# Kernel tuning notes

Hardware: AMD Instinct MI355X
Metric: run time of the kernel (lower is better)

Reference implementation:

```python
import jax, jax.numpy as jnp
import numpy as np

DIM = 1024
N_HEAD = 16
N_KV_HEAD = 4
HEAD_DIM = DIM // N_HEAD  # 64
INTER = 2688
B, N = 2, 2048
EPS = 1e-6


def setup_inputs() -> dict:
    key = jax.random.key(0)
    ks = jax.random.split(key, 10)
    std = 0.02
    x = jax.random.normal(ks[0], (B, N, DIM), dtype=jnp.float32)
    # rotary embedding: theta = pos * 10000^(-2i/d), cos/sin of shape [N, HEAD_DIM//2]
    inv_freq = 1.0 / (10000.0 ** (np.arange(0, HEAD_DIM, 2, dtype=np.float32) / HEAD_DIM))
    t = np.arange(N, dtype=np.float32)
    ang = np.outer(t, inv_freq)  # [N, HEAD_DIM//2]
    rope_cos = jnp.asarray(np.cos(ang))
    rope_sin = jnp.asarray(np.sin(ang))
    mask = jnp.tril(jnp.ones((N, N), dtype=bool))  # True = attend
    return {
        "x": x,
        "w_attn_norm": jnp.ones((DIM,), jnp.float32),
        "w_ffn_norm": jnp.ones((DIM,), jnp.float32),
        "Wq": jax.random.normal(ks[1], (DIM, N_HEAD * HEAD_DIM), jnp.float32) * std,
        "Wkv": jax.random.normal(ks[2], (DIM, 2 * N_KV_HEAD * HEAD_DIM), jnp.float32) * std,
        "Wo": jax.random.normal(ks[3], (N_HEAD * HEAD_DIM, DIM), jnp.float32) * std,
        "W1": jax.random.normal(ks[4], (DIM, INTER), jnp.float32) * std,
        "W2": jax.random.normal(ks[5], (INTER, DIM), jnp.float32) * std,
        "W3": jax.random.normal(ks[6], (DIM, INTER), jnp.float32) * std,
        "rope_cos": rope_cos,
        "rope_sin": rope_sin,
        "mask": mask,
    }


def _rms_norm(x, w):
    # nn.functional.rms_norm: x / sqrt(mean(x^2) + eps) * w
    return x * jax.lax.rsqrt(jnp.mean(x * x, axis=-1, keepdims=True) + EPS) * w


def _apply_rope(x, cos, sin):
    # x: [b, n, h, d]; consecutive pairs (x[2k], x[2k+1]) form complex numbers
    xr = x[..., 0::2]
    xi = x[..., 1::2]
    c = cos[None, :, None, :]
    s = sin[None, :, None, :]
    yr = xr * c - xi * s
    yi = xr * s + xi * c
    return jnp.stack([yr, yi], axis=-1).reshape(x.shape)


def _block(x, w_attn_norm, w_ffn_norm, Wq, Wkv, Wo, W1, W2, W3, rope_cos, rope_sin, mask):
    b, n, _ = x.shape
    # --- attention (GQA, use_cache=False prefill) ---
    h = _rms_norm(x, w_attn_norm)
    q = (h @ Wq).reshape(b, n, N_HEAD, HEAD_DIM)
    kv = h @ Wkv
    k, v = jnp.split(kv, 2, axis=-1)
    k = k.reshape(b, n, N_KV_HEAD, HEAD_DIM)
    v = v.reshape(b, n, N_KV_HEAD, HEAD_DIM)
    q = _apply_rope(q, rope_cos, rope_sin)
    k = _apply_rope(k, rope_cos, rope_sin)
    # einops repeat 'b n h d -> b n (r h) d' == tile along head axis
    r = N_HEAD // N_KV_HEAD
    k = jnp.tile(k, (1, 1, r, 1))
    v = jnp.tile(v, (1, 1, r, 1))
    scale = HEAD_DIM ** -0.5
    scores = jnp.einsum('bnhd,bmhd->bhnm', q, k) * scale
    scores = jnp.where(mask[None, None, :, :], scores, jnp.finfo(scores.dtype).min)
    attn = jax.nn.softmax(scores, axis=-1)
    o = jnp.einsum('bhnm,bmhd->bnhd', attn, v).reshape(b, n, N_HEAD * HEAD_DIM)
    x = x + o @ Wo
    # --- SwiGLU MLP ---
    h2 = _rms_norm(x, w_ffn_norm)
    ff = (jax.nn.silu(h2 @ W1) * (h2 @ W3)) @ W2
    return x + ff


def reference(x, w_attn_norm, w_ffn_norm, Wq, Wkv, Wo, W1, W2, W3, rope_cos, rope_sin, mask):
    return _block(x, w_attn_norm, w_ffn_norm, Wq, Wkv, Wo, W1, W2, W3, rope_cos, rope_sin, mask)
```

## Files before the change

kernel.cpp:

```cpp
#include <hip/hip_runtime.h>

#define DIM 1024
#define NH 16
#define NKV 4
#define HD 64
#define INTER 2688
#define BB 2
#define NN 2048
#define MM (BB*NN)

typedef __attribute__((ext_vector_type(4))) float f32x4;
typedef __attribute__((ext_vector_type(16))) float f32x16;
typedef __attribute__((ext_vector_type(8))) short short8;

#define CROW(r,h) ((((r)&3)) + 8*((r)>>2) + 4*(h))

__device__ __forceinline__ unsigned short f2bf(float f) {
  union { float f; unsigned u; } v; v.f = f;
  unsigned r = v.u + 0x7fffu + ((v.u >> 16) & 1u);
  return (unsigned short)(r >> 16);
}
__device__ __forceinline__ float bf2f(unsigned short u) {
  union { unsigned u; float f; } v; v.u = ((unsigned)u) << 16; return v.f;
}
__device__ __forceinline__ float ld_res(const float* p) { return *p; }
__device__ __forceinline__ float ld_res(const unsigned short* p) { return bf2f(*p); }
__device__ __forceinline__ void st_out(float* p, float v) { *p = v; }
__device__ __forceinline__ void st_out(unsigned short* p, float v) { *p = f2bf(v); }

__device__ __forceinline__ void glds16(const unsigned short* g, unsigned short* l) {
  __builtin_amdgcn_global_load_lds(
      (const __attribute__((address_space(1))) void*)g,
      (__attribute__((address_space(3))) void*)l, 16, 0, 0);
}

__device__ __forceinline__ void xcd_map(int& bx, int& by) {
  int gx = gridDim.x;
  int nwg = gx * gridDim.y;
  int bid = (int)blockIdx.y * gx + (int)blockIdx.x;
  int cpx = nwg >> 3;
  int lg = (bid & 7) * cpx + (bid >> 3);
  bx = lg % gx;
  by = lg / gx;
}

__global__ void transpose_all(const float* __restrict__ Wq, const float* __restrict__ Wkv,
                              const float* __restrict__ Wo, const float* __restrict__ W1,
                              const float* __restrict__ W3, const float* __restrict__ W2,
                              unsigned short* __restrict__ WqkvT, unsigned short* __restrict__ WoT,
                              unsigned short* __restrict__ W1T, unsigned short* __restrict__ W3T,
                              unsigned short* __restrict__ W2T) {
  int tb = blockIdx.x;
  const float* src; unsigned short* dst; int K, Nc, t0;
  if (tb < 1024)        { src = Wq;  dst = WqkvT;                         K = 1024; Nc = 1024; t0 = tb; }
  else if (tb < 1536)   { src = Wkv; dst = WqkvT + (size_t)1024 * 1024;   K = 1024; Nc = 512;  t0 = tb - 1024; }
  else if (tb < 2560)   { src = Wo;  dst = WoT;                           K = 1024; Nc = 1024; t0 = tb - 1536; }
  else if (tb < 5248)   { src = W1;  dst = W1T;                           K = 1024; Nc = 2688; t0 = tb - 2560; }
  else if (tb < 7936)   { src = W3;  dst = W3T;                           K = 1024; Nc = 2688; t0 = tb - 5248; }
  else                  { src = W2;  dst = W2T;                           K = 2688; Nc = 1024; t0 = tb - 7936; }
  int ntx = Nc >> 5;
  int n0 = (t0 % ntx) * 32, k0 = (t0 / ntx) * 32;
  __shared__ float tile[32][33];
  int tx = threadIdx.x & 31, ty = threadIdx.x >> 5;
#pragma unroll
  for (int i = 0; i < 32; i += 8)
    tile[ty + i][tx] = src[(size_t)(k0 + ty + i) * Nc + n0 + tx];
  __syncthreads();
#pragma unroll
  for (int i = 0; i < 32; i += 8)
    dst[(size_t)(n0 + ty + i) * K + k0 + tx] = f2bf(tile[tx][ty + i]);
}

template <typename InT>
__global__ void rmsnorm_k(const InT* __restrict__ x, const float* __restrict__ w,
                          unsigned short* __restrict__ h) {
  int row = blockIdx.x;
  int t = threadIdx.x;
  float4 v;
  if constexpr (sizeof(InT) == 4) {
    v = ((const float4*)(x + (size_t)row * DIM))[t];
  } else {
    ushort4 u = ((const ushort4*)(x + (size_t)row * DIM))[t];
    v.x = bf2f(u.x); v.y = bf2f(u.y); v.z = bf2f(u.z); v.w = bf2f(u.w);
  }
  float ss = v.x * v.x + v.y * v.y + v.z * v.z + v.w * v.w;
#pragma unroll
  for (int o = 1; o < 64; o <<= 1) ss += __shfl_xor(ss, o);
  __shared__ float ps[4];
  if ((t & 63) == 0) ps[t >> 6] = ss;
  __syncthreads();
  float r = rsqrtf((ps[0] + ps[1] + ps[2] + ps[3]) * (1.0f / DIM) + 1e-6f);
  float4 wv = ((const float4*)w)[t];
  ushort4 o4;
  o4.x = f2bf(v.x * r * wv.x);
  o4.y = f2bf(v.y * r * wv.y);
  o4.z = f2bf(v.z * r * wv.z);
  o4.w = f2bf(v.w * r * wv.w);
  *(ushort4*)(h + (size_t)row * DIM + t * 4) = o4;
}

template <typename ResT, typename OutT>
__global__ __launch_bounds__(256, 3) void gemm64(
    const unsigned short* __restrict__ A, const unsigned short* __restrict__ Bt,
    const ResT* __restrict__ res, OutT* __restrict__ C, int Nc, int K) {
  __shared__ __align__(16) unsigned short Asm[2][64 * 64];
  __shared__ __align__(16) unsigned short Bsm[2][128 * 64];
  int tid = threadIdx.x;
  int w = tid >> 6, l = tid & 63;
  int bx, by;
  xcd_map(bx, by);
  int bm = by * 64, bn = bx * 128;
  int wc = w * 32;
  int c0 = l & 15, g = l >> 4;

  int sra = w * 16 + (l >> 3);
  int srb = w * 32 + (l >> 3);
  int schA = ((l & 7) ^ (l >> 3)) * 8;
  const unsigned short* gA = A + (size_t)(bm + sra) * K + schA;
  const unsigned short* gB = Bt + (size_t)(bn + srb) * K + schA;
  int lsa = (w * 16) * 64, lsb = (w * 32) * 64;

  f32x4 acc[4][2] = {};
  int T = K / 64;
  glds16(gA, &Asm[0][lsa]);
  glds16(gA + 8 * K, &Asm[0][lsa + 8 * 64]);
  glds16(gB, &Bsm[0][lsb]);
  glds16(gB + 8 * K, &Bsm[0][lsb + 8 * 64]);
  glds16(gB + 16 * K, &Bsm[0][lsb + 16 * 64]);
  glds16(gB + 24 * K, &Bsm[0][lsb + 24 * 64]);
  __syncthreads();
  int buf = 0;
  for (int s = 0; s < T; ++s) {
    int nb = buf ^ 1;
    if (s + 1 < T) {
      int ko = (s + 1) * 64;
      glds16(gA + ko, &Asm[nb][lsa]);
      glds16(gA + 8 * K + ko, &Asm[nb][lsa + 8 * 64]);
      glds16(gB + ko, &Bsm[nb][lsb]);
      glds16(gB + 8 * K + ko, &Bsm[nb][lsb + 8 * 64]);
      glds16(gB + 16 * K + ko, &Bsm[nb][lsb + 16 * 64]);
      glds16(gB + 24 * K + ko, &Bsm[nb][lsb + 24 * 64]);
    }
    const unsigned short* As = Asm[buf];
    const unsigned short* Bs = Bsm[buf];
#pragma unroll
    for (int ks = 0; ks < 2; ++ks) {
      short8 af[4], bf[2];
#pragma unroll
      for (int m = 0; m < 4; m++) {
        int ra = m * 16 + c0;
        af[m] = *(const short8*)&As[ra * 64 + (((ks * 4 + g) ^ (ra & 7)) * 8)];
      }
#pragma unroll
      for (int n = 0; n < 2; n++) {
        int rb = wc + n * 16 + c0;
        bf[n] = *(const short8*)&Bs[rb * 64 + (((ks * 4 + g) ^ (rb & 7)) * 8)];
      }
      __builtin_amdgcn_s_setprio(1);
#pragma unroll
      for (int m = 0; m < 4; m++)
#pragma unroll
        for (int n = 0; n < 2; n++)
          acc[m][n] = __builtin_amdgcn_mfma_f32_16x16x32_bf16(af[m], bf[n], acc[m][n], 0, 0, 0);
      __builtin_amdgcn_s_setprio(0);
    }
    __syncthreads();
    buf = nb;
  }
  int gq = l >> 4;
#pragma unroll
  for (int m = 0; m < 4; m++) {
#pragma unroll
    for (int i = 0; i < 4; i++) {
      int row = bm + m * 16 + gq * 4 + i;
#pragma unroll
      for (int n = 0; n < 2; n++) {
        int col = bn + wc + n * 16 + c0;
        float v = acc[m][n][i] + ld_res(&res[(size_t)row * Nc + col]);
        st_out(&C[(size_t)row * Nc + col], v);
      }
    }
  }
}

__global__ __launch_bounds__(256, 3) void gemm_qkv(
    const unsigned short* __restrict__ A, const unsigned short* __restrict__ Bt,
    const float* __restrict__ cosb, const float* __restrict__ sinb,
    unsigned short* __restrict__ qb, unsigned short* __restrict__ kb,
    unsigned short* __restrict__ vtb) {
  const int K = 1024;
  const float QS = 0.125f * 1.44269504f;
  __shared__ __align__(16) unsigned short Asm[2][64 * 64];
  __shared__ __align__(16) unsigned short Bsm[2][128 * 64];
  int tid = threadIdx.x;
  int w = tid >> 6, l = tid & 63;
  int bx, by;
  xcd_map(bx, by);
  int bm = by * 64, bn = bx * 128;
  int wc = w * 32;
  int c0 = l & 15, g = l >> 4;

  int sra = w * 16 + (l >> 3);
  int srb = w * 32 + (l >> 3);
  int schA = ((l & 7) ^ (l >> 3)) * 8;
  const unsigned short* gA = A + (size_t)(bm + sra) * K + schA;
  const unsigned short* gB = Bt + (size_t)(bn + srb) * K + schA;
  int lsa = (w * 16) * 64, lsb = (w * 32) * 64;

  f32x4 acc[4][2] = {};
  int T = K / 64;
  glds16(gA, &Asm[0][lsa]);
  glds16(gA + 8 * K, &Asm[0][lsa + 8 * 64]);
  glds16(gB, &Bsm[0][lsb]);
  glds16(gB + 8 * K, &Bsm[0][lsb + 8 * 64]);
  glds16(gB + 16 * K, &Bsm[0][lsb + 16 * 64]);
  glds16(gB + 24 * K, &Bsm[0][lsb + 24 * 64]);
  __syncthreads();
  int buf = 0;
  for (int s = 0; s < T; ++s) {
    int nb = buf ^ 1;
    if (s + 1 < T) {
      int ko = (s + 1) * 64;
      glds16(gA + ko, &Asm[nb][lsa]);
      glds16(gA + 8 * K + ko, &Asm[nb][lsa + 8 * 64]);
      glds16(gB + ko, &Bsm[nb][lsb]);
      glds16(gB + 8 * K + ko, &Bsm[nb][lsb + 8 * 64]);
      glds16(gB + 16 * K + ko, &Bsm[nb][lsb + 16 * 64]);
      glds16(gB + 24 * K + ko, &Bsm[nb][lsb + 24 * 64]);
    }
    const unsigned short* As = Asm[buf];
    const unsigned short* Bs = Bsm[buf];
#pragma unroll
    for (int ks = 0; ks < 2; ++ks) {
      short8 af[4], bf[2];
#pragma unroll
      for (int m = 0; m < 4; m++) {
        int ra = m * 16 + c0;
        af[m] = *(const short8*)&As[ra * 64 + (((ks * 4 + g) ^ (ra & 7)) * 8)];
      }
#pragma unroll
      for (int n = 0; n < 2; n++) {
        int rb = wc + n * 16 + c0;
        bf[n] = *(const short8*)&Bs[rb * 64 + (((ks * 4 + g) ^ (rb & 7)) * 8)];
      }
      __builtin_amdgcn_s_setprio(1);
#pragma unroll
      for (int m = 0; m < 4; m++)
#pragma unroll
        for (int n = 0; n < 2; n++)
          acc[m][n] = __builtin_amdgcn_mfma_f32_16x16x32_bf16(af[m], bf[n], acc[m][n], 0, 0, 0);
      __builtin_amdgcn_s_setprio(0);
    }
    __syncthreads();
    buf = nb;
  }
  int gq = l >> 4;
  int lodd = c0 & 1;
#pragma unroll
  for (int m = 0; m < 4; m++) {
#pragma unroll
    for (int i = 0; i < 4; i++) {
      int row = bm + m * 16 + gq * 4 + i;
      int b = row >> 11, tok = row & (NN - 1);
#pragma unroll
      for (int n = 0; n < 2; n++) {
        int col = bn + wc + n * 16 + c0;
        float val = acc[m][n][i];
        float partner = __shfl_xor(val, 1);
        if (bn < 1024) {
          int head = col >> 6, d = col & 63, j = d >> 1;
          float c = cosb[tok * 32 + j], s = sinb[tok * 32 + j];
          float r = lodd ? (partner * s + val * c) : (val * c - partner * s);
          qb[(((size_t)(b * NH + head)) * NN + tok) * 64 + d] = f2bf(r * QS);
        } else if (bn < 1280) {
          int cc = col - 1024;
          int kvh = cc >> 6, d = cc & 63, j = d >> 1;
          float c = cosb[tok * 32 + j], s = sinb[tok * 32 + j];
          float r = lodd ? (partner * s + val * c) : (val * c - partner * s);
          kb[(((size_t)(b * NKV + kvh)) * NN + tok) * 64 + d] = f2bf(r);
        } else {
          int cc = col - 1280;
          int kvh = cc >> 6, d = cc & 63;
          vtb[(((size_t)(b * NKV + kvh)) * 64 + d) * NN + tok] = f2bf(val);
        }
      }
    }
  }
}

__global__ __launch_bounds__(256, 4) void gemm_ffn13(
    const unsigned short* __restrict__ A, const unsigned short* __restrict__ B1t,
    const unsigned short* __restrict__ B3t, unsigned short* __restrict__ G,
    int Nc, int K) {
  __shared__ __align__(16) unsigned short Asm[2 * 128 * 32];
  __shared__ __align__(16) unsigned short B1sm[2 * 64 * 32];
  __shared__ __align__(16) unsigned short B3sm[2 * 64 * 32];
  int tid = threadIdx.x;
  int w = tid >> 6, l = tid & 63;
  int bm = blockIdx.y * 128, bn = blockIdx.x * 64;
  int wr = (w >> 1) * 64, wc = (w & 1) * 32;
  int c0 = l & 15, g = l >> 4;

  int sr = w * 32 + (l >> 2);
  int sb = w * 16 + (l >> 2);
  int sc  = ((l & 3) ^ ((sr >> 1) & 3)) * 8;
  int scb = ((l & 3) ^ ((sb >> 1) & 3)) * 8;
  const unsigned short* gA0 = A + (size_t)(bm + sr) * K + sc;
  const unsigned short* gA1 = A + (size_t)(bm + sr + 16) * K + sc;
  const unsigned short* gB1 = B1t + (size_t)(bn + sb) * K + scb;
  const unsigned short* gB3 = B3t + (size_t)(bn + sb) * K + scb;
  int ls0 = (w * 32) * 32, ls1 = (w * 32 + 16) * 32, lsb = (w * 16) * 32;

  int aoff[4], boff[2];
#pragma unroll
  for (int m = 0; m < 4; m++) {
    int ra = wr + m * 16 + c0;
    aoff[m] = ra * 32 + (g ^ ((ra >> 1) & 3)) * 8;
  }
#pragma unroll
  for (int n = 0; n < 2; n++) {
    int rb = wc + n * 16 + c0;
    boff[n] = rb * 32 + (g ^ ((rb >> 1) & 3)) * 8;
  }

  f32x4 a1[4][2] = {};
  f32x4 a3[4][2] = {};
  int nsteps = K / 32;
  glds16(gA0, &Asm[ls0]);
  glds16(gA1, &Asm[ls1]);
  glds16(gB1, &B1sm[lsb]);
  glds16(gB3, &B3sm[lsb]);
  __syncthreads();
  int buf = 0;
  for (int s = 0; s < nsteps; ++s) {
    int nb = buf ^ 1;
    if (s + 1 < nsteps) {
      int ko = (s + 1) * 32;
      glds16(gA0 + ko, &Asm[nb * 4096 + ls0]);
      glds16(gA1 + ko, &Asm[nb * 4096 + ls1]);
      glds16(gB1 + ko, &B1sm[nb * 2048 + lsb]);
      glds16(gB3 + ko, &B3sm[nb * 2048 + lsb]);
    }
    const unsigned short* As = &Asm[buf * 4096];
    const unsigned short* B1s = &B1sm[buf * 2048];
    const unsigned short* B3s = &B3sm[buf * 2048];
    short8 af[4], b1f[2], b3f[2];
#pragma unroll
    for (int m = 0; m < 4; m++) af[m] = *(const short8*)&As[aoff[m]];
#pragma unroll
    for (int n = 0; n < 2; n++) {
      b1f[n] = *(const short8*)&B1s[boff[n]];
      b3f[n] = *(const short8*)&B3s[boff[n]];
    }
    __builtin_amdgcn_s_setprio(1);
#pragma unroll
    for (int m = 0; m < 4; m++)
#pragma unroll
      for (int n = 0; n < 2; n++) {
        a1[m][n] = __builtin_amdgcn_mfma_f32_16x16x32_bf16(af[m], b1f[n], a1[m][n], 0, 0, 0);
        a3[m][n] = __builtin_amdgcn_mfma_f32_16x16x32_bf16(af[m], b3f[n], a3[m][n], 0, 0, 0);
      }
    __builtin_amdgcn_s_setprio(0);
    __syncthreads();
    buf = nb;
  }
  int gq = l >> 4;
#pragma unroll
  for (int m = 0; m < 4; m++) {
#pragma unroll
    for (int i = 0; i < 4; i++) {
      int row = bm + wr + m * 16 + gq * 4 + i;
#pragma unroll
      for (int n = 0; n < 2; n++) {
        int col = bn + wc + n * 16 + c0;
        float x1 = a1[m][n][i], x3 = a3[m][n][i];
        float sg = x1 / (1.0f + __expf(-x1));
        G[(size_t)row * Nc + col] = f2bf(sg * x3);
      }
    }
  }
}

__global__ __launch_bounds__(256, 3) void attn_k(
    const unsigned short* __restrict__ qg_, const unsigned short* __restrict__ kg_,
    const unsigned short* __restrict__ vg_, unsigned short* __restrict__ ob) {
  __shared__ __align__(16) unsigned short Ksm[2][64 * 64];
  __shared__ __align__(16) unsigned short Vsm[2][64 * 64];
  int qb = (blockIdx.z == 0) ? (int)blockIdx.x : ((int)gridDim.x - 1 - (int)blockIdx.x);
  int h = blockIdx.y, b = blockIdx.z;
  int kvh = h & 3;
  int tid = threadIdx.x, w = tid >> 6, l = tid & 63;
  int q5 = l & 31, hi = l >> 5;
  int qwbase = qb * 128 + w * 32;
  int qgl = qwbase + q5;

  const unsigned short* Kg = kg_ + ((size_t)(b * NKV + kvh)) * NN * 64;
  const unsigned short* Vg = vg_ + ((size_t)(b * NKV + kvh)) * 64 * NN;

  short8 qf[4];
  {
    const unsigned short* qrow = qg_ + (((size_t)(b * NH + h)) * NN + qgl) * 64 + hi * 8;
#pragma unroll
    for (int d = 0; d < 4; d++) qf[d] = *(const short8*)(qrow + d * 16);
  }

  int srow = l >> 3;
  int schunk = (l & 7) ^ (srow & 7);
  const unsigned short* gK = Kg + (size_t)(w * 16 + srow) * 64 + schunk * 8;
  const unsigned short* gV = Vg + (size_t)(w * 16 + srow) * NN + schunk * 8;

  int nkt = qb * 2 + 2;
  int nkt_w = ((qwbase + 31) >> 6) + 1;

  f32x16 O0 = {}, O1 = {};
  float m_r = -1e30f, l_r = 0.0f;

  glds16(gK, &Ksm[0][w * 1024]);
  glds16(gK + 8 * 64, &Ksm[0][w * 1024 + 512]);
  glds16(gV, &Vsm[0][w * 1024]);
  glds16(gV + 8 * NN, &Vsm[0][w * 1024 + 512]);
  __syncthreads();

  int buf = 0;
  for (int kt = 0; kt < nkt; ++kt) {
    int n0 = kt * 64;
    if (kt + 1 < nkt) {
      int nb = buf ^ 1;
      glds16(gK + (size_t)(n0 + 64) * 64, &Ksm[nb][w * 1024]);
      glds16(gK + (size_t)(n0 + 64) * 64 + 8 * 64, &Ksm[nb][w * 1024 + 512]);
      glds16(gV + n0 + 64, &Vsm[nb][w * 1024]);
      glds16(gV + 8 * NN + n0 + 64, &Vsm[nb][w * 1024 + 512]);
    }
    if (kt < nkt_w) {
      const unsigned short* Ks = Ksm[buf];
      const unsigned short* Vs = Vsm[buf];
      f32x16 S[2];
      __builtin_amdgcn_s_setprio(1);
#pragma unroll
      for (int s = 0; s < 2; s++) {
        f32x16 acc = {};
        int row = s * 32 + q5;
#pragma unroll
        for (int d = 0; d < 4; d++) {
          int ch = (2 * d + hi) ^ (row & 7);
          short8 kf = *(const short8*)&Ks[row * 64 + ch * 8];
          acc = __builtin_amdgcn_mfma_f32_32x32x16_bf16(kf, qf[d], acc, 0, 0, 0);
        }
        S[s] = acc;
      }
      __builtin_amdgcn_s_setprio(0);
      if (kt == nkt_w - 1) {
#pragma unroll
        for (int s = 0; s < 2; s++)
#pragma unroll
          for (int r = 0; r < 16; r++) {
            int kg = n0 + s * 32 + CROW(r, hi);
            S[s][r] = (kg > qgl) ? -1e30f : S[s][r];
          }
      }
      float t16[16];
#pragma unroll
      for (int r = 0; r < 16; r++) t16[r] = fmaxf(S[0][r], S[1][r]);
#pragma unroll
      for (int k = 8; k >= 1; k >>= 1)
#pragma unroll
        for (int r = 0; r < k; r++) t16[r] = fmaxf(t16[r], t16[r + k]);
      float pm = fmaxf(t16[0], __shfl_xor(t16[0], 32));
      if (!__all(pm <= m_r + 8.0f)) {
        float mn = fmaxf(m_r, pm);
        float alpha = exp2f(m_r - mn);
        m_r = mn;
        l_r *= alpha;
        float ab[16];
#pragma unroll
        for (int r = 0; r < 16; r++) ab[r] = __shfl(alpha, CROW(r, 0) + 4 * hi);
#pragma unroll
        for (int r = 0; r < 16; r++) { O0[r] *= ab[r]; O1[r] *= ab[r]; }
      }
#pragma unroll
      for (int s = 0; s < 2; s++)
#pragma unroll
        for (int r = 0; r < 16; r++) S[s][r] = exp2f(S[s][r] - m_r);
      float u[16];
#pragma unroll
      for (int r = 0; r < 16; r++) u[r] = S[0][r] + S[1][r];
#pragma unroll
      for (int k = 8; k >= 1; k >>= 1)
#pragma unroll
        for (int r = 0; r < k; r++) u[r] += u[r + k];
      l_r += (u[0] + __shfl_xor(u[0], 32));
      short8 paf[4];
#pragma unroll
      for (int ks = 0; ks < 4; ks++) {
        const int s = ks >> 1, e = ks & 1;
        unsigned a0, a1, b0, b1;
        asm("v_cvt_pk_bf16_f32 %0, %1, %2" : "=v"(a0) : "v"(S[s][8*e+0]), "v"(S[s][8*e+1]));
        asm("v_cvt_pk_bf16_f32 %0, %1, %2" : "=v"(a1) : "v"(S[s][8*e+2]), "v"(S[s][8*e+3]));
        asm("v_cvt_pk_bf16_f32 %0, %1, %2" : "=v"(b0) : "v"(S[s][8*e+4]), "v"(S[s][8*e+5]));
        asm("v_cvt_pk_bf16_f32 %0, %1, %2" : "=v"(b1) : "v"(S[s][8*e+6]), "v"(S[s][8*e+7]));
        asm("v_permlane32_swap_b32 %0, %1" : "+v"(a0), "+v"(b0));
        asm("v_permlane32_swap_b32 %0, %1" : "+v"(a1), "+v"(b1));
        union { unsigned u4[4]; short8 s8; } pk;
        pk.u4[0] = a0; pk.u4[1] = a1; pk.u4[2] = b0; pk.u4[3] = b1;
        paf[ks] = pk.s8;
      }
      __builtin_amdgcn_s_setprio(1);
#pragma unroll
      for (int ks = 0; ks < 4; ks++) {
        int row0 = q5, row1 = 32 + q5;
        short8 vf0 = *(const short8*)&Vs[row0 * 64 + (((2 * ks + hi) ^ (row0 & 7)) * 8)];
        short8 vf1 = *(const short8*)&Vs[row1 * 64 + (((2 * ks + hi) ^ (row1 & 7)) * 8)];
        O0 = __builtin_amdgcn_mfma_f32_32x32x16_bf16(paf[ks], vf0, O0, 0, 0, 0);
        O1 = __builtin_amdgcn_mfma_f32_32x32x16_bf16(paf[ks], vf1, O1, 0, 0, 0);
      }
      __builtin_amdgcn_s_setprio(0);
    }
    __syncthreads();
    buf ^= 1;
  }
  float linv = 1.0f / l_r;
  float lb[16];
#pragma unroll
  for (int r = 0; r < 16; r++) lb[r] = __shfl(linv, CROW(r, 0) + 4 * hi);
#pragma unroll
  for (int r = 0; r < 16; r++) {
    int orow = qwbase + CROW(r, hi);
    size_t base = ((size_t)b * NN + orow) * 1024 + h * 64 + q5;
    ob[base] = f2bf(O0[r] * lb[r]);
    ob[base + 32] = f2bf(O1[r] * lb[r]);
  }
}

extern "C" void kernel_launch(void* const* d_in, const int* in_sizes, int n_in,
                              void* d_out, int out_size, void* d_ws, size_t ws_size,
                              hipStream_t stream) {
  (void)in_sizes; (void)n_in; (void)out_size; (void)ws_size;
  const float* x    = (const float*)d_in[0];
  const float* w_an = (const float*)d_in[1];
  const float* w_fn = (const float*)d_in[2];
  const float* Wq   = (const float*)d_in[3];
  const float* Wkv  = (const float*)d_in[4];
  const float* Wo   = (const float*)d_in[5];
  const float* W1   = (const float*)d_in[6];
  const float* W2   = (const float*)d_in[7];
  const float* W3   = (const float*)d_in[8];
  const float* cosb = (const float*)d_in[9];
  const float* sinb = (const float*)d_in[10];
  float* out = (float*)d_out;

  char* ws = (char*)d_ws;
  size_t off = 0;
  auto take = [&](size_t bytes) {
    size_t r = off;
    off += (bytes + 255) & ~(size_t)255;
    return r;
  };
  unsigned short* WqkvT = (unsigned short*)(ws + take((size_t)1536 * 1024 * 2));
  unsigned short* WoT   = (unsigned short*)(ws + take((size_t)1024 * 1024 * 2));
  unsigned short* W1T   = (unsigned short*)(ws + take((size_t)2688 * 1024 * 2));
  unsigned short* W3T   = (unsigned short*)(ws + take((size_t)2688 * 1024 * 2));
  unsigned short* W2T   = (unsigned short*)(ws + take((size_t)2688 * 1024 * 2));
  unsigned short* hA    = (unsigned short*)(ws + take((size_t)MM * DIM * 2));
  unsigned short* gbuf  = (unsigned short*)(ws + take((size_t)MM * INTER * 2));
  unsigned short* qbuf = (unsigned short*)(ws + take((size_t)MM * DIM * 2));
  unsigned short* kbuf = (unsigned short*)(ws + take((size_t)BB * NKV * NN * HD * 2));
  unsigned short* vtb  = (unsigned short*)(ws + take((size_t)BB * NKV * NN * HD * 2));
  unsigned short* obuf = (unsigned short*)(ws + take((size_t)MM * DIM * 2));
  unsigned short* x2b  = (unsigned short*)(ws + take((size_t)MM * DIM * 2));

  transpose_all<<<10624, 256, 0, stream>>>(Wq, Wkv, Wo, W1, W3, W2,
                                           WqkvT, WoT, W1T, W3T, W2T);
  rmsnorm_k<float><<<MM, 256, 0, stream>>>(x, w_an, hA);
  gemm_qkv<<<dim3(1536 / 128, MM / 64), 256, 0, stream>>>(hA, WqkvT, cosb, sinb,
                                                          qbuf, kbuf, vtb);
  attn_k<<<dim3(NN / 128, NH, BB), 256, 0, stream>>>(qbuf, kbuf, vtb, obuf);
  gemm64<float, unsigned short><<<dim3(1024 / 128, MM / 64), 256, 0, stream>>>(
      obuf, WoT, x, x2b, 1024, 1024);
  rmsnorm_k<unsigned short><<<MM, 256, 0, stream>>>(x2b, w_fn, hA);
  gemm_ffn13<<<dim3(INTER / 64, MM / 128), 256, 0, stream>>>(hA, W1T, W3T, gbuf, INTER, 1024);
  gemm64<unsigned short, float><<<dim3(1024 / 128, MM / 64), 256, 0, stream>>>(
      gbuf, W2T, x2b, out, 1024, 2688);
}
```

Measured before the change: 221.3 us.

## Deepen FFN13 GEMM K-tile to 64 with XCD-aware block swizzle

Doubles the K depth of each shared-memory stage in the fused W1/W3 GEMM from 32 to 64, which halves the number of barriers and loop iterations, and uses an 8-way XOR swizzle for the wider rows. Blocks are remapped so that consecutive block IDs, which are spread across XCDs, land on neighbouring tiles within each XCD, with the aim of better L2 reuse. LDS use doubles, so launch bounds drop to 2 blocks per SM and occupancy falls. The remap hardcodes a 42x32 grid.

```diff
diff --git a/kernel.cpp b/kernel.cpp
--- a/kernel.cpp
+++ b/kernel.cpp
@@ -288,79 +288,83 @@
   }
 }
 
-__global__ __launch_bounds__(256, 4) void gemm_ffn13(
+__global__ __launch_bounds__(256, 2) void gemm_ffn13(
     const unsigned short* __restrict__ A, const unsigned short* __restrict__ B1t,
     const unsigned short* __restrict__ B3t, unsigned short* __restrict__ G,
     int Nc, int K) {
-  __shared__ __align__(16) unsigned short Asm[2 * 128 * 32];
-  __shared__ __align__(16) unsigned short B1sm[2 * 64 * 32];
-  __shared__ __align__(16) unsigned short B3sm[2 * 64 * 32];
+  __shared__ __align__(16) unsigned short Asm[2][128 * 64];
+  __shared__ __align__(16) unsigned short B1sm[2][64 * 64];
+  __shared__ __align__(16) unsigned short B3sm[2][64 * 64];
   int tid = threadIdx.x;
   int w = tid >> 6, l = tid & 63;
-  int bm = blockIdx.y * 128, bn = blockIdx.x * 64;
+  int bid = (int)blockIdx.y * gridDim.x + (int)blockIdx.x;
+  int xcd = bid & 7, rr = bid >> 3;
+  int bx = (xcd & 1) * 21 + (rr >> 3);
+  int by = (xcd >> 1) * 8 + (rr & 7);
+  int bm = by * 128, bn = bx * 64;
   int wr = (w >> 1) * 64, wc = (w & 1) * 32;
   int c0 = l & 15, g = l >> 4;
 
-  int sr = w * 32 + (l >> 2);
-  int sb = w * 16 + (l >> 2);
-  int sc  = ((l & 3) ^ ((sr >> 1) & 3)) * 8;
-  int scb = ((l & 3) ^ ((sb >> 1) & 3)) * 8;
-  const unsigned short* gA0 = A + (size_t)(bm + sr) * K + sc;
-  const unsigned short* gA1 = A + (size_t)(bm + sr + 16) * K + sc;
-  const unsigned short* gB1 = B1t + (size_t)(bn + sb) * K + scb;
-  const unsigned short* gB3 = B3t + (size_t)(bn + sb) * K + scb;
-  int ls0 = (w * 32) * 32, ls1 = (w * 32 + 16) * 32, lsb = (w * 16) * 32;
-
-  int aoff[4], boff[2];
-#pragma unroll
-  for (int m = 0; m < 4; m++) {
-    int ra = wr + m * 16 + c0;
-    aoff[m] = ra * 32 + (g ^ ((ra >> 1) & 3)) * 8;
-  }
-#pragma unroll
-  for (int n = 0; n < 2; n++) {
-    int rb = wc + n * 16 + c0;
-    boff[n] = rb * 32 + (g ^ ((rb >> 1) & 3)) * 8;
-  }
+  int lr = l >> 3;
+  int sch = ((l & 7) ^ lr) * 8;
+  const unsigned short* gA  = A + (size_t)(bm + w * 32 + lr) * K + sch;
+  const unsigned short* gB1 = B1t + (size_t)(bn + w * 16 + lr) * K + sch;
+  const unsigned short* gB3 = B3t + (size_t)(bn + w * 16 + lr) * K + sch;
+  int lsA = (w * 32) * 64, lsB = (w * 16) * 64;
 
   f32x4 a1[4][2] = {};
   f32x4 a3[4][2] = {};
-  int nsteps = K / 32;
-  glds16(gA0, &Asm[ls0]);
-  glds16(gA1, &Asm[ls1]);
-  glds16(gB1, &B1sm[lsb]);
-  glds16(gB3, &B3sm[lsb]);
+  int T = K / 64;
+  glds16(gA, &Asm[0][lsA]);
+  glds16(gA + 8 * K, &Asm[0][lsA + 8 * 64]);
+  glds16(gA + 16 * K, &Asm[0][lsA + 16 * 64]);
+  glds16(gA + 24 * K, &Asm[0][lsA + 24 * 64]);
+  glds16(gB1, &B1sm[0][lsB]);
+  glds16(gB1 + 8 * K, &B1sm[0][lsB + 8 * 64]);
+  glds16(gB3, &B3sm[0][lsB]);
+  glds16(gB3 + 8 * K, &B3sm[0][lsB + 8 * 64]);
   __syncthreads();
   int buf = 0;
-  for (int s = 0; s < nsteps; ++s) {
+  for (int s = 0; s < T; ++s) {
     int nb = buf ^ 1;
-    if (s + 1 < nsteps) {
-      int ko = (s + 1) * 32;
-      glds16(gA0 + ko, &Asm[nb * 4096 + ls0]);
-      glds16(gA1 + ko, &Asm[nb * 4096 + ls1]);
-      glds16(gB1 + ko, &B1sm[nb * 2048 + lsb]);
-      glds16(gB3 + ko, &B3sm[nb * 2048 + lsb]);
-    }
-    const unsigned short* As = &Asm[buf * 4096];
-    const unsigned short* B1s = &B1sm[buf * 2048];
-    const unsigned short* B3s = &B3sm[buf * 2048];
-    short8 af[4], b1f[2], b3f[2];
-#pragma unroll
-    for (int m = 0; m < 4; m++) af[m] = *(const short8*)&As[aoff[m]];
-#pragma unroll
-    for (int n = 0; n < 2; n++) {
-      b1f[n] = *(const short8*)&B1s[boff[n]];
-      b3f[n] = *(const short8*)&B3s[boff[n]];
-    }
-    __builtin_amdgcn_s_setprio(1);
-#pragma unroll
-    for (int m = 0; m < 4; m++)
+    if (s + 1 < T) {
+      int ko = (s + 1) * 64;
+      glds16(gA + ko, &Asm[nb][lsA]);
+      glds16(gA + 8 * K + ko, &Asm[nb][lsA + 8 * 64]);
+      glds16(gA + 16 * K + ko, &Asm[nb][lsA + 16 * 64]);
+      glds16(gA + 24 * K + ko, &Asm[nb][lsA + 24 * 64]);
+      glds16(gB1 + ko, &B1sm[nb][lsB]);
+      glds16(gB1 + 8 * K + ko, &B1sm[nb][lsB + 8 * 64]);
+      glds16(gB3 + ko, &B3sm[nb][lsB]);
+      glds16(gB3 + 8 * K + ko, &B3sm[nb][lsB + 8 * 64]);
+    }
+    const unsigned short* As = Asm[buf];
+    const unsigned short* B1s = B1sm[buf];
+    const unsigned short* B3s = B3sm[buf];
+#pragma unroll
+    for (int ks = 0; ks < 2; ++ks) {
+      short8 af[4], b1f[2], b3f[2];
+#pragma unroll
+      for (int m = 0; m < 4; m++) {
+        int ra = wr + m * 16 + c0;
+        af[m] = *(const short8*)&As[ra * 64 + (((ks * 4 + g) ^ (ra & 7)) * 8)];
+      }
 #pragma unroll
       for (int n = 0; n < 2; n++) {
-        a1[m][n] = __builtin_amdgcn_mfma_f32_16x16x32_bf16(af[m], b1f[n], a1[m][n], 0, 0, 0);
-        a3[m][n] = __builtin_amdgcn_mfma_f32_16x16x32_bf16(af[m], b3f[n], a3[m][n], 0, 0, 0);
-      }
-    __builtin_amdgcn_s_setprio(0);
+        int rb = wc + n * 16 + c0;
+        b1f[n] = *(const short8*)&B1s[rb * 64 + (((ks * 4 + g) ^ (rb & 7)) * 8)];
+        b3f[n] = *(const short8*)&B3s[rb * 64 + (((ks * 4 + g) ^ (rb & 7)) * 8)];
+      }
+      __builtin_amdgcn_s_setprio(1);
+#pragma unroll
+      for (int m = 0; m < 4; m++)
+#pragma unroll
+        for (int n = 0; n < 2; n++) {
+          a1[m][n] = __builtin_amdgcn_mfma_f32_16x16x32_bf16(af[m], b1f[n], a1[m][n], 0, 0, 0);
+          a3[m][n] = __builtin_amdgcn_mfma_f32_16x16x32_bf16(af[m], b3f[n], a3[m][n], 0, 0, 0);
+        }
+      __builtin_amdgcn_s_setprio(0);
+    }
     __syncthreads();
     buf = nb;
   }
```

Result: faster. 216.6 us, median of 3 (-2.1%).

## Restructure FFN W1/W3 GEMM with 128x128 tiles, triple buffering and XCD-aware block mapping

Applied to the files above, without the earlier changes.

Rewrites the fused W1/W3 SwiGLU GEMM to use 512-thread blocks with 128x128 output tiles and a K-step of 64. The K loop uses a three-stage LDS ring with asynchronous global-to-LDS loads issued between the MFMA phases. A 1D grid is remapped so that consecutive row tiles land on the same XCD, which should improve L2 reuse of A. The goal is to hide load latency and raise arithmetic intensity, at the cost of about 144KB of LDS per block, hand-written waitcnt and barrier sequencing, and lower occupancy.

```diff
diff --git a/kernel.cpp b/kernel.cpp
--- a/kernel.cpp
+++ b/kernel.cpp
@@ -288,91 +288,151 @@
   }
 }
 
-__global__ __launch_bounds__(256, 4) void gemm_ffn13(
+__global__ __launch_bounds__(512, 2) void gemm_ffn13(
     const unsigned short* __restrict__ A, const unsigned short* __restrict__ B1t,
     const unsigned short* __restrict__ B3t, unsigned short* __restrict__ G,
     int Nc, int K) {
-  __shared__ __align__(16) unsigned short Asm[2 * 128 * 32];
-  __shared__ __align__(16) unsigned short B1sm[2 * 64 * 32];
-  __shared__ __align__(16) unsigned short B3sm[2 * 64 * 32];
+  __shared__ __align__(16) unsigned short Asm[3][128 * 64];
+  __shared__ __align__(16) unsigned short B1sm[3][128 * 64];
+  __shared__ __align__(16) unsigned short B3sm[3][128 * 64];
   int tid = threadIdx.x;
   int w = tid >> 6, l = tid & 63;
-  int bm = blockIdx.y * 128, bn = blockIdx.x * 64;
-  int wr = (w >> 1) * 64, wc = (w & 1) * 32;
+  int bid = (int)blockIdx.x;
+  int xcd = bid & 7, r = bid >> 3;
+  int bx = r >> 2, by = (xcd << 2) + (r & 3);
+  int bm = by * 128, bn = bx * 128;
+  int wm = w >> 2, wn = w & 3;
   int c0 = l & 15, g = l >> 4;
 
-  int sr = w * 32 + (l >> 2);
-  int sb = w * 16 + (l >> 2);
-  int sc  = ((l & 3) ^ ((sr >> 1) & 3)) * 8;
-  int scb = ((l & 3) ^ ((sb >> 1) & 3)) * 8;
-  const unsigned short* gA0 = A + (size_t)(bm + sr) * K + sc;
-  const unsigned short* gA1 = A + (size_t)(bm + sr + 16) * K + sc;
-  const unsigned short* gB1 = B1t + (size_t)(bn + sb) * K + scb;
-  const unsigned short* gB3 = B3t + (size_t)(bn + sb) * K + scb;
-  int ls0 = (w * 32) * 32, ls1 = (w * 32 + 16) * 32, lsb = (w * 16) * 32;
-
-  int aoff[4], boff[2];
-#pragma unroll
-  for (int m = 0; m < 4; m++) {
-    int ra = wr + m * 16 + c0;
-    aoff[m] = ra * 32 + (g ^ ((ra >> 1) & 3)) * 8;
-  }
-#pragma unroll
-  for (int n = 0; n < 2; n++) {
-    int rb = wc + n * 16 + c0;
-    boff[n] = rb * 32 + (g ^ ((rb >> 1) & 3)) * 8;
-  }
+  int lr = l >> 3;
+  int sch = ((l & 7) ^ lr) * 8;
+  const unsigned short* gA  = A   + (size_t)(bm + w * 16 + lr) * K + sch;
+  const unsigned short* gB1 = B1t + (size_t)(bn + w * 16 + lr) * K + sch;
+  const unsigned short* gB3 = B3t + (size_t)(bn + w * 16 + lr) * K + sch;
+  int ls = (w * 16) * 64;
 
   f32x4 a1[4][2] = {};
   f32x4 a3[4][2] = {};
-  int nsteps = K / 32;
-  glds16(gA0, &Asm[ls0]);
-  glds16(gA1, &Asm[ls1]);
-  glds16(gB1, &B1sm[lsb]);
-  glds16(gB3, &B3sm[lsb]);
-  __syncthreads();
-  int buf = 0;
-  for (int s = 0; s < nsteps; ++s) {
-    int nb = buf ^ 1;
-    if (s + 1 < nsteps) {
-      int ko = (s + 1) * 32;
-      glds16(gA0 + ko, &Asm[nb * 4096 + ls0]);
-      glds16(gA1 + ko, &Asm[nb * 4096 + ls1]);
-      glds16(gB1 + ko, &B1sm[nb * 2048 + lsb]);
-      glds16(gB3 + ko, &B3sm[nb * 2048 + lsb]);
-    }
-    const unsigned short* As = &Asm[buf * 4096];
-    const unsigned short* B1s = &B1sm[buf * 2048];
-    const unsigned short* B3s = &B3sm[buf * 2048];
-    short8 af[4], b1f[2], b3f[2];
-#pragma unroll
-    for (int m = 0; m < 4; m++) af[m] = *(const short8*)&As[aoff[m]];
+  const int T = K / 64;
+
+#pragma unroll
+  for (int p = 0; p < 2; ++p) {
+    int ko = p * 64;
+    glds16(gA + ko, &Asm[p][ls]);
+    glds16(gA + 8 * K + ko, &Asm[p][ls + 512]);
+    glds16(gB1 + ko, &B1sm[p][ls]);
+    glds16(gB1 + 8 * K + ko, &B1sm[p][ls + 512]);
+    glds16(gB3 + ko, &B3sm[p][ls]);
+    glds16(gB3 + 8 * K + ko, &B3sm[p][ls + 512]);
+  }
+  asm volatile("s_waitcnt vmcnt(6)" ::: "memory");
+  asm volatile("s_barrier" ::: "memory");
+
+  int cur = 0;
+  for (int t = 0; t < T; ++t) {
+    int nx = cur + 2; if (nx >= 3) nx -= 3;
+    bool pre = (t + 2 < T);
+    int ko = (t + 2) * 64;
+    const unsigned short* As  = Asm[cur];
+    const unsigned short* B1s = B1sm[cur];
+    const unsigned short* B3s = B3sm[cur];
+    short8 af[4], bf[2];
+
+#pragma unroll
+    for (int m = 0; m < 4; m++) {
+      int ra = wm * 64 + m * 16 + c0;
+      af[m] = *(const short8*)&As[ra * 64 + ((g ^ (ra & 7)) * 8)];
+    }
 #pragma unroll
     for (int n = 0; n < 2; n++) {
-      b1f[n] = *(const short8*)&B1s[boff[n]];
-      b3f[n] = *(const short8*)&B3s[boff[n]];
-    }
+      int rb = wn * 32 + n * 16 + c0;
+      bf[n] = *(const short8*)&B1s[rb * 64 + ((g ^ (rb & 7)) * 8)];
+    }
+    if (pre) { glds16(gA + ko, &Asm[nx][ls]); glds16(gA + 8 * K + ko, &Asm[nx][ls + 512]); }
+    asm volatile("s_barrier" ::: "memory");
+    asm volatile("s_waitcnt lgkmcnt(0)" ::: "memory");
+    __builtin_amdgcn_sched_barrier(0);
     __builtin_amdgcn_s_setprio(1);
 #pragma unroll
     for (int m = 0; m < 4; m++)
 #pragma unroll
+      for (int n = 0; n < 2; n++)
+        a1[m][n] = __builtin_amdgcn_mfma_f32_16x16x32_bf16(af[m], bf[n], a1[m][n], 0, 0, 0);
+    __builtin_amdgcn_s_setprio(0);
+
+#pragma unroll
+    for (int n = 0; n < 2; n++) {
+      int rb = wn * 32 + n * 16 + c0;
+      bf[n] = *(const short8*)&B3s[rb * 64 + ((g ^ (rb & 7)) * 8)];
+    }
+    if (pre) { glds16(gB1 + ko, &B1sm[nx][ls]); glds16(gB1 + 8 * K + ko, &B1sm[nx][ls + 512]); }
+    asm volatile("s_barrier" ::: "memory");
+    asm volatile("s_waitcnt lgkmcnt(0)" ::: "memory");
+    __builtin_amdgcn_sched_barrier(0);
+    __builtin_amdgcn_s_setprio(1);
+#pragma unroll
+    for (int m = 0; m < 4; m++)
+#pragma unroll
+      for (int n = 0; n < 2; n++)
+        a3[m][n] = __builtin_amdgcn_mfma_f32_16x16x32_bf16(af[m], bf[n], a3[m][n], 0, 0, 0);
+    __builtin_amdgcn_s_setprio(0);
+
+#pragma unroll
+    for (int m = 0; m < 4; m++) {
+      int ra = wm * 64 + m * 16 + c0;
+      af[m] = *(const short8*)&As[ra * 64 + (((4 + g) ^ (ra & 7)) * 8)];
+    }
+#pragma unroll
+    for (int n = 0; n < 2; n++) {
+      int rb = wn * 32 + n * 16 + c0;
+      bf[n] = *(const short8*)&B1s[rb * 64 + (((4 + g) ^ (rb & 7)) * 8)];
+    }
+    if (pre) { glds16(gB3 + ko, &B3sm[nx][ls]); glds16(gB3 + 8 * K + ko, &B3sm[nx][ls + 512]); }
+    asm volatile("s_barrier" ::: "memory");
+    asm volatile("s_waitcnt lgkmcnt(0)" ::: "memory");
+    __builtin_amdgcn_sched_barrier(0);
+    __builtin_amdgcn_s_setprio(1);
+#pragma unroll
+    for (int m = 0; m < 4; m++)
+#pragma unroll
+      for (int n = 0; n < 2; n++)
+        a1[m][n] = __builtin_amdgcn_mfma_f32_16x16x32_bf16(af[m], bf[n], a1[m][n], 0, 0, 0);
+    __builtin_amdgcn_s_setprio(0);
+
+#pragma unroll
+    for (int n = 0; n < 2; n++) {
+      int rb = wn * 32 + n * 16 + c0;
+      bf[n] = *(const short8*)&B3s[rb * 64 + (((4 + g) ^ (rb & 7)) * 8)];
+    }
+    asm volatile("s_barrier" ::: "memory");
+    asm volatile("s_waitcnt lgkmcnt(0)" ::: "memory");
+    __builtin_amdgcn_sched_barrier(0);
+    __builtin_amdgcn_s_setprio(1);
+#pragma unroll
+    for (int m = 0; m < 4; m++)
+#pragma unroll
+      for (int n = 0; n < 2; n++)
+        a3[m][n] = __builtin_amdgcn_mfma_f32_16x16x32_bf16(af[m], bf[n], a3[m][n], 0, 0, 0);
+    __builtin_amdgcn_s_setprio(0);
+
+    if (pre) {
+      asm volatile("s_waitcnt vmcnt(6)" ::: "memory");
+    } else if (t + 2 == T) {
+      asm volatile("s_waitcnt vmcnt(0)" ::: "memory");
+    }
+    if (t + 1 < T) asm volatile("s_barrier" ::: "memory");
+    cur = cur + 1 == 3 ? 0 : cur + 1;
+  }
+
+  int gq = l >> 4;
+#pragma unroll
+  for (int m = 0; m < 4; m++) {
+#pragma unroll
+    for (int i = 0; i < 4; i++) {
+      int row = bm + wm * 64 + m * 16 + gq * 4 + i;
+#pragma unroll
       for (int n = 0; n < 2; n++) {
-        a1[m][n] = __builtin_amdgcn_mfma_f32_16x16x32_bf16(af[m], b1f[n], a1[m][n], 0, 0, 0);
-        a3[m][n] = __builtin_amdgcn_mfma_f32_16x16x32_bf16(af[m], b3f[n], a3[m][n], 0, 0, 0);
-      }
-    __builtin_amdgcn_s_setprio(0);
-    __syncthreads();
-    buf = nb;
-  }
-  int gq = l >> 4;
-#pragma unroll
-  for (int m = 0; m < 4; m++) {
-#pragma unroll
-    for (int i = 0; i < 4; i++) {
-      int row = bm + wr + m * 16 + gq * 4 + i;
-#pragma unroll
-      for (int n = 0; n < 2; n++) {
-        int col = bn + wc + n * 16 + c0;
+        int col = bn + wn * 32 + n * 16 + c0;
         float x1 = a1[m][n][i], x3 = a3[m][n][i];
         float sg = x1 / (1.0f + __expf(-x1));
         G[(size_t)row * Nc + col] = f2bf(sg * x3);
@@ -577,7 +637,7 @@
   gemm64<float, unsigned short><<<dim3(1024 / 128, MM / 64), 256, 0, stream>>>(
       obuf, WoT, x, x2b, 1024, 1024);
   rmsnorm_k<unsigned short><<<MM, 256, 0, stream>>>(x2b, w_fn, hA);
-  gemm_ffn13<<<dim3(INTER / 64, MM / 128), 256, 0, stream>>>(hA, W1T, W3T, gbuf, INTER, 1024);
+  gemm_ffn13<<<672, 512, 0, stream>>>(hA, W1T, W3T, gbuf, INTER, 1024);
   gemm64<unsigned short, float><<<dim3(1024 / 128, MM / 64), 256, 0, stream>>>(
       gbuf, W2T, x2b, out, 1024, 2688);
 }
```

After: 235.2 us. +6.3%, slower.

## Enlarge fused W1/W3 GEMM tile to 128x128 with eight waves per block

Applied to the files above, without the earlier changes.

The SwiGLU up-projection GEMM block tile grows from 128x64 to 128x128 columns and runs 512 threads (8 waves) in a 2x4 wave grid instead of 256 threads. Each wave keeps the same 64x32 output sub-tile, and the shared-memory load pattern is simplified so every thread issues one 16-byte copy each for A, B1 and B3. This halves the number of blocks that reload the A tile and raises reuse of the staged activations. In exchange LDS per block grows to 48KB, the launch bound of 512x4 may not be reachable, and the grid shrinks to 21x32 blocks, which may reduce wave-level parallelism and tail balance.

```diff
diff --git a/kernel.cpp b/kernel.cpp
--- a/kernel.cpp
+++ b/kernel.cpp
@@ -288,62 +288,57 @@
   }
 }
 
-__global__ __launch_bounds__(256, 4) void gemm_ffn13(
+__global__ __launch_bounds__(512, 4) void gemm_ffn13(
     const unsigned short* __restrict__ A, const unsigned short* __restrict__ B1t,
     const unsigned short* __restrict__ B3t, unsigned short* __restrict__ G,
     int Nc, int K) {
-  __shared__ __align__(16) unsigned short Asm[2 * 128 * 32];
-  __shared__ __align__(16) unsigned short B1sm[2 * 64 * 32];
-  __shared__ __align__(16) unsigned short B3sm[2 * 64 * 32];
+  __shared__ __align__(16) unsigned short Asm[2][128 * 32];
+  __shared__ __align__(16) unsigned short B1sm[2][128 * 32];
+  __shared__ __align__(16) unsigned short B3sm[2][128 * 32];
   int tid = threadIdx.x;
   int w = tid >> 6, l = tid & 63;
-  int bm = blockIdx.y * 128, bn = blockIdx.x * 64;
-  int wr = (w >> 1) * 64, wc = (w & 1) * 32;
+  int bm = blockIdx.y * 128, bn = blockIdx.x * 128;
+  int wm = w >> 2, wn = w & 3;
   int c0 = l & 15, g = l >> 4;
 
-  int sr = w * 32 + (l >> 2);
-  int sb = w * 16 + (l >> 2);
-  int sc  = ((l & 3) ^ ((sr >> 1) & 3)) * 8;
-  int scb = ((l & 3) ^ ((sb >> 1) & 3)) * 8;
-  const unsigned short* gA0 = A + (size_t)(bm + sr) * K + sc;
-  const unsigned short* gA1 = A + (size_t)(bm + sr + 16) * K + sc;
-  const unsigned short* gB1 = B1t + (size_t)(bn + sb) * K + scb;
-  const unsigned short* gB3 = B3t + (size_t)(bn + sb) * K + scb;
-  int ls0 = (w * 32) * 32, ls1 = (w * 32 + 16) * 32, lsb = (w * 16) * 32;
+  int sr = w * 16 + (l >> 2);
+  int sc = ((l & 3) ^ ((sr >> 1) & 3)) * 8;
+  const unsigned short* gA  = A   + (size_t)(bm + sr) * K + sc;
+  const unsigned short* gB1 = B1t + (size_t)(bn + sr) * K + sc;
+  const unsigned short* gB3 = B3t + (size_t)(bn + sr) * K + sc;
+  int ls = (w * 16) * 32;
 
   int aoff[4], boff[2];
 #pragma unroll
   for (int m = 0; m < 4; m++) {
-    int ra = wr + m * 16 + c0;
+    int ra = wm * 64 + m * 16 + c0;
     aoff[m] = ra * 32 + (g ^ ((ra >> 1) & 3)) * 8;
   }
 #pragma unroll
   for (int n = 0; n < 2; n++) {
-    int rb = wc + n * 16 + c0;
+    int rb = wn * 32 + n * 16 + c0;
     boff[n] = rb * 32 + (g ^ ((rb >> 1) & 3)) * 8;
   }
 
   f32x4 a1[4][2] = {};
   f32x4 a3[4][2] = {};
   int nsteps = K / 32;
-  glds16(gA0, &Asm[ls0]);
-  glds16(gA1, &Asm[ls1]);
-  glds16(gB1, &B1sm[lsb]);
-  glds16(gB3, &B3sm[lsb]);
+  glds16(gA, &Asm[0][ls]);
+  glds16(gB1, &B1sm[0][ls]);
+  glds16(gB3, &B3sm[0][ls]);
   __syncthreads();
   int buf = 0;
   for (int s = 0; s < nsteps; ++s) {
     int nb = buf ^ 1;
     if (s + 1 < nsteps) {
       int ko = (s + 1) * 32;
-      glds16(gA0 + ko, &Asm[nb * 4096 + ls0]);
-      glds16(gA1 + ko, &Asm[nb * 4096 + ls1]);
-      glds16(gB1 + ko, &B1sm[nb * 2048 + lsb]);
-      glds16(gB3 + ko, &B3sm[nb * 2048 + lsb]);
-    }
-    const unsigned short* As = &Asm[buf * 4096];
-    const unsigned short* B1s = &B1sm[buf * 2048];
-    const unsigned short* B3s = &B3sm[buf * 2048];
+      glds16(gA + ko, &Asm[nb][ls]);
+      glds16(gB1 + ko, &B1sm[nb][ls]);
+      glds16(gB3 + ko, &B3sm[nb][ls]);
+    }
+    const unsigned short* As = Asm[buf];
+    const unsigned short* B1s = B1sm[buf];
+    const unsigned short* B3s = B3sm[buf];
     short8 af[4], b1f[2], b3f[2];
 #pragma unroll
     for (int m = 0; m < 4; m++) af[m] = *(const short8*)&As[aoff[m]];
@@ -369,10 +364,10 @@
   for (int m = 0; m < 4; m++) {
 #pragma unroll
     for (int i = 0; i < 4; i++) {
-      int row = bm + wr + m * 16 + gq * 4 + i;
+      int row = bm + wm * 64 + m * 16 + gq * 4 + i;
 #pragma unroll
       for (int n = 0; n < 2; n++) {
-        int col = bn + wc + n * 16 + c0;
+        int col = bn + wn * 32 + n * 16 + c0;
         float x1 = a1[m][n][i], x3 = a3[m][n][i];
         float sg = x1 / (1.0f + __expf(-x1));
         G[(size_t)row * Nc + col] = f2bf(sg * x3);
@@ -577,7 +572,7 @@
   gemm64<float, unsigned short><<<dim3(1024 / 128, MM / 64), 256, 0, stream>>>(
       obuf, WoT, x, x2b, 1024, 1024);
   rmsnorm_k<unsigned short><<<MM, 256, 0, stream>>>(x2b, w_fn, hA);
-  gemm_ffn13<<<dim3(INTER / 64, MM / 128), 256, 0, stream>>>(hA, W1T, W3T, gbuf, INTER, 1024);
+  gemm_ffn13<<<dim3(INTER / 128, MM / 128), 512, 0, stream>>>(hA, W1T, W3T, gbuf, INTER, 1024);
   gemm64<unsigned short, float><<<dim3(1024 / 128, MM / 64), 256, 0, stream>>>(
       gbuf, W2T, x2b, out, 1024, 2688);
 }
```

Result: no change. 225.1 us (+1.7%).
